# Kernel optimization log

Measured on AMD Instinct MI355X. Metric: run time of the kernel, lower is better.

Reference implementation:

```python
import jax, jax.numpy as jnp
import numpy as np

B, SQ, SK, D, H, DFF = 4, 1024, 1024, 1024, 16, 4096
DEPTH = D // H
EPS = 1e-6


def setup_inputs() -> dict:
    key = jax.random.key(0)
    ks = jax.random.split(key, 32)
    s = 0.02
    inp = {
        "x": jax.random.normal(ks[0], (B, SQ, D), jnp.float32),
        "enc_output": jax.random.normal(ks[1], (B, SK, D), jnp.float32),
        # causal look-ahead mask: 1 where attention is disallowed
        "look_ahead_mask": (1.0 - jnp.tril(jnp.ones((SQ, SQ), jnp.float32)))[None, None],
        "padding_mask": jnp.zeros((B, 1, 1, SK), jnp.float32),
    }
    names = ["wq1", "wk1", "wv1", "wo1", "wq2", "wk2", "wv2", "wo2"]
    for i, n in enumerate(names):
        inp[n] = jax.random.normal(ks[2 + i], (D, D), jnp.float32) * s
        inp["b" + n[1:]] = jnp.zeros((D,), jnp.float32)
    inp["w_ffn1"] = jax.random.normal(ks[12], (D, DFF), jnp.float32) * s
    inp["b_ffn1"] = jnp.zeros((DFF,), jnp.float32)
    inp["w_ffn2"] = jax.random.normal(ks[13], (DFF, D), jnp.float32) * s
    inp["b_ffn2"] = jnp.zeros((D,), jnp.float32)
    for i in (1, 2, 3):
        inp[f"gamma{i}"] = jnp.ones((D,), jnp.float32)
        inp[f"beta{i}"] = jnp.zeros((D,), jnp.float32)
    return inp


def _layernorm(x, gamma, beta):
    mu = jnp.mean(x, axis=-1, keepdims=True)
    var = jnp.var(x, axis=-1, keepdims=True)
    return (x - mu) * jax.lax.rsqrt(var + EPS) * gamma + beta


def _split_heads(x):
    b, s, _ = x.shape
    return x.reshape(b, s, H, DEPTH).transpose(0, 2, 1, 3)  # (B,H,S,depth)


def _mha(v_in, k_in, q_in, mask, wq, bq, wk, bk, wv, bv, wo, bo):
    q = _split_heads(q_in @ wq + bq)
    k = _split_heads(k_in @ wk + bk)
    v = _split_heads(v_in @ wv + bv)
    logits = jnp.einsum("bhqd,bhkd->bhqk", q, k) / jnp.sqrt(jnp.float32(DEPTH))
    if mask is not None:
        logits = logits + mask * -1e9
    attn = jax.nn.softmax(logits, axis=-1)
    out = jnp.einsum("bhqk,bhkd->bhqd", attn, v)
    out = out.transpose(0, 2, 1, 3).reshape(q_in.shape[0], -1, D)
    return out @ wo + bo, attn


def reference(x, enc_output, look_ahead_mask, padding_mask,
              wq1, bq1, wk1, bk1, wv1, bv1, wo1, bo1,
              wq2, bq2, wk2, bk2, wv2, bv2, wo2, bo2,
              w_ffn1, b_ffn1, w_ffn2, b_ffn2,
              gamma1, beta1, gamma2, beta2, gamma3, beta3):
    attn1, aw1 = _mha(x, x, x, look_ahead_mask,
                      wq1, bq1, wk1, bk1, wv1, bv1, wo1, bo1)
    out1 = _layernorm(attn1 + x, gamma1, beta1)
    attn2, aw2 = _mha(enc_output, enc_output, out1, padding_mask,
                      wq2, bq2, wk2, bk2, wv2, bv2, wo2, bo2)
    out2 = _layernorm(attn2 + out1, gamma2, beta2)
    ffn = jax.nn.relu(out2 @ w_ffn1 + b_ffn1) @ w_ffn2 + b_ffn2
    out3 = _layernorm(ffn + out2, gamma3, beta3)
    return out3, aw1, aw2
```

## Files before the change

kernel.cpp:

```cpp
#include <hip/hip_runtime.h>

#define NB 4
#define SEQ 1024
#define DM 1024
#define NH 16
#define DEP 64
#define DFFN 4096

typedef __attribute__((ext_vector_type(8))) short short8;
typedef __attribute__((ext_vector_type(4))) float f32x4;
typedef __attribute__((ext_vector_type(4))) unsigned short us4;

__device__ __forceinline__ unsigned short f2bf(float f) {
    union { float f; unsigned int u; } v; v.f = f;
    unsigned int u = v.u;
    return (unsigned short)((u + 0x7FFFu + ((u >> 16) & 1u)) >> 16);
}

__device__ __forceinline__ void gload16(const void* g, void* l) {
    __builtin_amdgcn_global_load_lds((const __attribute__((address_space(1))) unsigned int*)g,
                                     (__attribute__((address_space(3))) unsigned int*)l, 16, 0, 0);
}

__global__ __launch_bounds__(256) void cast2_kernel(const float* __restrict__ a,
                                                    const float* __restrict__ b,
                                                    unsigned short* __restrict__ oa,
                                                    unsigned short* __restrict__ ob, int n4) {
    int i = blockIdx.x * 256 + threadIdx.x;
    const float* in = blockIdx.y ? b : a;
    unsigned short* out = blockIdx.y ? ob : oa;
    if (i < n4) {
        float4 f = ((const float4*)in)[i];
        us4 u;
        u[0] = f2bf(f.x); u[1] = f2bf(f.y); u[2] = f2bf(f.z); u[3] = f2bf(f.w);
        ((us4*)out)[i] = u;
    }
}

__global__ __launch_bounds__(256) void castT_kernel(const float* __restrict__ in,
                                                    unsigned short* __restrict__ out,
                                                    int R, int C) {
    __shared__ float tile[64][65];
    const int t = threadIdx.x;
    const int c0 = blockIdx.x * 64, r0 = blockIdx.y * 64;
#pragma unroll
    for (int p = 0; p < 4; ++p) {
        int r = p * 16 + (t >> 4), c = (t & 15) * 4;
        float4 f = *(const float4*)(in + (size_t)(r0 + r) * C + c0 + c);
        tile[r][c] = f.x; tile[r][c + 1] = f.y; tile[r][c + 2] = f.z; tile[r][c + 3] = f.w;
    }
    __syncthreads();
#pragma unroll
    for (int p = 0; p < 4; ++p) {
        int n = p * 16 + (t >> 4), k = (t & 15) * 4;
        us4 u;
#pragma unroll
        for (int j = 0; j < 4; ++j) u[j] = f2bf(tile[k + j][n]);
        *(us4*)(out + (size_t)(c0 + n) * R + r0 + k) = u;
    }
}

struct P8 { const float* p[8]; };
__global__ __launch_bounds__(256) void castT8_kernel(P8 srcs, unsigned short* __restrict__ dstbase) {
    __shared__ float tile[64][65];
    const float* in = srcs.p[blockIdx.z];
    unsigned short* out = dstbase + (size_t)blockIdx.z * DM * DM;
    const int t = threadIdx.x;
    const int c0 = blockIdx.x * 64, r0 = blockIdx.y * 64;
#pragma unroll
    for (int p = 0; p < 4; ++p) {
        int r = p * 16 + (t >> 4), c = (t & 15) * 4;
        float4 f = *(const float4*)(in + (size_t)(r0 + r) * DM + c0 + c);
        tile[r][c] = f.x; tile[r][c + 1] = f.y; tile[r][c + 2] = f.z; tile[r][c + 3] = f.w;
    }
    __syncthreads();
#pragma unroll
    for (int p = 0; p < 4; ++p) {
        int n = p * 16 + (t >> 4), k = (t & 15) * 4;
        us4 u;
#pragma unroll
        for (int j = 0; j < 4; ++j) u[j] = f2bf(tile[k + j][n]);
        *(us4*)(out + (size_t)(c0 + n) * DM + r0 + k) = u;
    }
}

__global__ __launch_bounds__(256) void biaspack_kernel(const float* __restrict__ bq1,
                                                       const float* __restrict__ bk1,
                                                       const float* __restrict__ bv1,
                                                       const float* __restrict__ bk2,
                                                       const float* __restrict__ bv2,
                                                       float* __restrict__ bqkv1,
                                                       float* __restrict__ bkv2) {
    int i = blockIdx.x * 256 + threadIdx.x;
    if (i < 1024) bqkv1[i] = bq1[i];
    else if (i < 2048) bqkv1[i] = bk1[i - 1024];
    else if (i < 3072) bqkv1[i] = bv1[i - 2048];
    else if (i < 4096) bkv2[i - 3072] = bk2[i - 3072];
    else if (i < 5120) bkv2[i - 3072] = bv2[i - 4096];
}

template <int BM, int BN, int BK, int KSPLIT, int RELU, int WB, int WF, int WVT>
__global__ __launch_bounds__(256) void gemm_kernel(const unsigned short* __restrict__ A,
                                                   const unsigned short* __restrict__ Wt,
                                                   const float* __restrict__ bias,
                                                   unsigned short* __restrict__ Cb,
                                                   float* __restrict__ Cf,
                                                   float* __restrict__ Cf2,
                                                   unsigned short* __restrict__ Vt,
                                                   int vstart,
                                                   int M, int N, int K) {
    constexpr int AM = BM / 32;
    constexpr int KS = BK / 32;
    constexpr int LPR = BK / 8;
    constexpr int RPI = 64 / LPR;
    constexpr int AR = (BM / 4) / RPI;
    constexpr int BR = (BN / 4) / RPI;
    __shared__ unsigned short As[BM * BK];
    __shared__ unsigned short Bs[BN * BK];
    const int t = threadIdx.x;
    const int lane = t & 63, w = t >> 6;
    const int m0 = blockIdx.y * BM, n0 = blockIdx.x * BN;
    const int wm = (w >> 1) * (BM / 2), wn = (w & 1) * (BN / 2);
    const int lr = lane & 15, g = lane >> 4, kb = g * 8;
    const int srow = lane / LPR, scol = (lane % LPR) * 8;
    const int kofs = (KSPLIT == 2 && blockIdx.z) ? K / 2 : 0;
    const int Keff = (KSPLIT == 2) ? K / 2 : K;

    f32x4 acc[AM][4];
#pragma unroll
    for (int a = 0; a < AM; ++a)
#pragma unroll
        for (int b = 0; b < 4; ++b)
#pragma unroll
            for (int j = 0; j < 4; ++j) acc[a][b][j] = 0.f;

    for (int kt = 0; kt < Keff; kt += BK) {
        __syncthreads();
#pragma unroll
        for (int ia = 0; ia < AR; ++ia) {
            int rb = w * (BM / 4) + ia * RPI;
            gload16(A + (size_t)(m0 + rb + srow) * K + kofs + kt + scol, As + rb * BK);
        }
#pragma unroll
        for (int ib = 0; ib < BR; ++ib) {
            int rb = w * (BN / 4) + ib * RPI;
            gload16(Wt + (size_t)(n0 + rb + srow) * K + kofs + kt + scol, Bs + rb * BK);
        }
        __syncthreads();

        short8 af[AM][KS], bfr[4][KS];
#pragma unroll
        for (int i = 0; i < AM; ++i)
#pragma unroll
            for (int ks = 0; ks < KS; ++ks)
                af[i][ks] = *(const short8*)&As[(wm + i * 16 + lr) * BK + ks * 32 + kb];
#pragma unroll
        for (int i = 0; i < 4; ++i)
#pragma unroll
            for (int ks = 0; ks < KS; ++ks)
                bfr[i][ks] = *(const short8*)&Bs[(wn + i * 16 + lr) * BK + ks * 32 + kb];
#pragma unroll
        for (int ks = 0; ks < KS; ++ks)
#pragma unroll
            for (int am = 0; am < AM; ++am)
#pragma unroll
                for (int bn = 0; bn < 4; ++bn)
                    acc[am][bn] = __builtin_amdgcn_mfma_f32_16x16x32_bf16(af[am][ks], bfr[bn][ks], acc[am][bn], 0, 0, 0);
    }

    float* cfo = (KSPLIT == 2 && blockIdx.z) ? Cf2 : Cf;
    const bool addb = bias && (KSPLIT == 1 || blockIdx.z == 0);
#pragma unroll
    for (int am = 0; am < AM; ++am) {
#pragma unroll
        for (int bn = 0; bn < 4; ++bn) {
            int col = n0 + wn + bn * 16 + lr;
            float bv = addb ? bias[col] : 0.f;
            int rowb = m0 + wm + am * 16 + g * 4;
            float vv[4];
#pragma unroll
            for (int i = 0; i < 4; ++i) {
                float v = acc[am][bn][i] + bv;
                if (RELU) v = v > 0.f ? v : 0.f;
                vv[i] = v;
                if (WF) cfo[(size_t)(rowb + i) * N + col] = v;
                if (WB) Cb[(size_t)(rowb + i) * N + col] = f2bf(v);
            }
            if (WVT && col >= vstart) {
                int h = (col - vstart) >> 6, dep = (col - vstart) & 63;
                int b = rowb >> 10, kpos = rowb & 1023;
                us4 u;
#pragma unroll
                for (int i = 0; i < 4; ++i) u[i] = f2bf(vv[i]);
                *(us4*)(Vt + ((size_t)(b * NH + h) * DEP + dep) * SEQ + kpos) = u;
            }
        }
    }
}

template <int CAUSAL>
__global__ __launch_bounds__(256, 2) void attn_kernel(const unsigned short* __restrict__ Q, int ldq,
                                                      const unsigned short* __restrict__ Kp, int ldk,
                                                      const unsigned short* __restrict__ Vt,
                                                      const float* __restrict__ pad,
                                                      float* __restrict__ aw,
                                                      unsigned short* __restrict__ ctx) {
    __shared__ unsigned short Ks[256 * 64];
    __shared__ unsigned short Pch[32 * 256];
    __shared__ float redm[4][32];
    __shared__ float reds[4][32];
    const int t = threadIdx.x, lane = t & 63, w = t >> 6;
    const int lr = lane & 15, g = lane >> 4;
    const int id = blockIdx.x;
    const int bh = (id & 7) + ((id >> 8) << 3);
    const int qt = (id >> 3) & 31;
    const int q0 = qt * 32;
    const int b = bh >> 4, h = bh & 15;
    const size_t qbase = (size_t)b * SEQ * ldq + (size_t)h * DEP;
    const size_t kbase = (size_t)b * SEQ * ldk + (size_t)h * DEP;
    const int kcmax = CAUSAL ? ((q0 + 16) >> 8) + 1 : 4;

    short8 aq[2][2];
#pragma unroll
    for (int p = 0; p < 2; ++p)
#pragma unroll
        for (int ks = 0; ks < 2; ++ks)
            aq[p][ks] = *(const short8*)(Q + qbase + (size_t)(q0 + p * 16 + lr) * ldq + ks * 32 + g * 8);

    f32x4 acc[2][4][4];
#pragma unroll
    for (int p = 0; p < 2; ++p)
#pragma unroll
        for (int a = 0; a < 4; ++a)
#pragma unroll
            for (int b2 = 0; b2 < 4; ++b2)
#pragma unroll
                for (int j = 0; j < 4; ++j) acc[p][a][b2][j] = 0.f;

    const int srow = lane >> 3;
    const int sslot = (lane & 7) ^ srow;

#pragma unroll
    for (int kc = 0; kc < 4; ++kc) {
        if (kc < kcmax) {
            __syncthreads();
#pragma unroll
            for (int i = 0; i < 8; ++i) {
                int rb = w * 64 + i * 8;
                gload16(Kp + kbase + (size_t)(kc * 256 + rb + srow) * ldk + sslot * 8,
                        Ks + rb * 64);
            }
            __syncthreads();
#pragma unroll
            for (int ks = 0; ks < 2; ++ks)
#pragma unroll
                for (int bn = 0; bn < 4; ++bn) {
                    int row = w * 64 + bn * 16 + lr;
                    short8 bk = *(const short8*)((const char*)Ks + row * 128 +
                                                 ((ks * 64 + g * 16) ^ ((lr & 7) << 4)));
                    acc[0][kc][bn] = __builtin_amdgcn_mfma_f32_16x16x32_bf16(bk, aq[0][ks], acc[0][kc][bn], 0, 0, 0);
                    acc[1][kc][bn] = __builtin_amdgcn_mfma_f32_16x16x32_bf16(bk, aq[1][ks], acc[1][kc][bn], 0, 0, 0);
                }
        }
    }

    float mrow[2] = {-1e30f, -1e30f};
#pragma unroll
    for (int kc = 0; kc < 4; ++kc) {
        if (kc < kcmax) {
#pragma unroll
            for (int bn = 0; bn < 4; ++bn) {
                int k4 = kc * 256 + w * 64 + bn * 16 + g * 4;
                f32x4 pv = {0.f, 0.f, 0.f, 0.f};
                if (pad) pv = *(const f32x4*)(pad + (size_t)b * SEQ + k4);
#pragma unroll
                for (int p = 0; p < 2; ++p) {
                    int q = q0 + p * 16 + lr;
#pragma unroll
                    for (int i = 0; i < 4; ++i) {
                        float v = acc[p][kc][bn][i] * 0.125f + pv[i] * -1e9f;
                        if (CAUSAL && (k4 + i) > q) v = -1e30f;
                        acc[p][kc][bn][i] = v;
                        mrow[p] = fmaxf(mrow[p], v);
                    }
                }
            }
        }
    }
#pragma unroll
    for (int p = 0; p < 2; ++p) {
        mrow[p] = fmaxf(mrow[p], __shfl_xor(mrow[p], 16));
        mrow[p] = fmaxf(mrow[p], __shfl_xor(mrow[p], 32));
    }
    if (lane < 16) { redm[w][lr] = mrow[0]; redm[w][16 + lr] = mrow[1]; }
    __syncthreads();
    float Mv[2];
#pragma unroll
    for (int p = 0; p < 2; ++p)
        Mv[p] = fmaxf(fmaxf(redm[0][p * 16 + lr], redm[1][p * 16 + lr]),
                      fmaxf(redm[2][p * 16 + lr], redm[3][p * 16 + lr]));

    float srw[2] = {0.f, 0.f};
#pragma unroll
    for (int kc = 0; kc < 4; ++kc) {
        if (kc < kcmax) {
#pragma unroll
            for (int p = 0; p < 2; ++p)
#pragma unroll
                for (int bn = 0; bn < 4; ++bn)
#pragma unroll
                    for (int i = 0; i < 4; ++i) {
                        float e = __expf(acc[p][kc][bn][i] - Mv[p]);
                        acc[p][kc][bn][i] = e;
                        srw[p] += e;
                    }
        }
    }
#pragma unroll
    for (int p = 0; p < 2; ++p) {
        srw[p] += __shfl_xor(srw[p], 16);
        srw[p] += __shfl_xor(srw[p], 32);
    }
    if (lane < 16) { reds[w][lr] = srw[0]; reds[w][16 + lr] = srw[1]; }
    __syncthreads();
    float inv[2];
#pragma unroll
    for (int p = 0; p < 2; ++p)
        inv[p] = 1.0f / (reds[0][p * 16 + lr] + reds[1][p * 16 + lr] +
                         reds[2][p * 16 + lr] + reds[3][p * 16 + lr]);

#pragma unroll
    for (int p = 0; p < 2; ++p) {
        float* awrow = aw + ((size_t)bh * SEQ + q0 + p * 16 + lr) * SEQ;
#pragma unroll
        for (int kc = 0; kc < 4; ++kc)
#pragma unroll
            for (int bn = 0; bn < 4; ++bn) {
                f32x4 o = {0.f, 0.f, 0.f, 0.f};
                if (kc < kcmax) {
#pragma unroll
                    for (int i = 0; i < 4; ++i) o[i] = acc[p][kc][bn][i] * inv[p];
                }
                *(f32x4*)(awrow + kc * 256 + w * 64 + bn * 16 + g * 4) = o;
            }
    }

    f32x4 acc2[2];
#pragma unroll
    for (int p = 0; p < 2; ++p)
#pragma unroll
        for (int j = 0; j < 4; ++j) acc2[p][j] = 0.f;
    char* pch = (char*)Pch;
    const int sw = (lr & 7) << 4;
#pragma unroll
    for (int kc = 0; kc < 4; ++kc) {
        if (kc < kcmax) {
            __syncthreads();
#pragma unroll
            for (int p = 0; p < 2; ++p)
#pragma unroll
                for (int bn = 0; bn < 4; ++bn) {
                    us4 u;
#pragma unroll
                    for (int i = 0; i < 4; ++i) u[i] = f2bf(acc[p][kc][bn][i] * inv[p]);
                    *(us4*)(pch + (p * 16 + lr) * 512 + ((w * 128 + bn * 32 + g * 8) ^ sw)) = u;
                }
            __syncthreads();
#pragma unroll
            for (int ks = 0; ks < 8; ++ks) {
                short8 bf = *(const short8*)(Vt + ((size_t)bh * DEP + w * 16 + lr) * SEQ + kc * 256 + ks * 32 + g * 8);
#pragma unroll
                for (int p = 0; p < 2; ++p) {
                    short8 af = *(const short8*)(pch + (p * 16 + lr) * 512 + ((ks * 64 + g * 16) ^ sw));
                    acc2[p] = __builtin_amdgcn_mfma_f32_16x16x32_bf16(af, bf, acc2[p], 0, 0, 0);
                }
            }
        }
    }
#pragma unroll
    for (int p = 0; p < 2; ++p)
#pragma unroll
        for (int i = 0; i < 4; ++i)
            ctx[((size_t)b * SEQ + q0 + p * 16 + g * 4 + i) * DM + h * DEP + w * 16 + lr] = f2bf(acc2[p][i]);
}

template <int WB, int X2EN>
__global__ __launch_bounds__(256) void ln_kernel(const float* __restrict__ X,
                                                 const float* __restrict__ X2,
                                                 const float* __restrict__ R,
                                                 const float* __restrict__ gamma,
                                                 const float* __restrict__ beta,
                                                 float* __restrict__ outF,
                                                 unsigned short* __restrict__ outB) {
    size_t row = blockIdx.x;
    const int t = threadIdx.x;
    float4 a = ((const float4*)(X + (row << 10)))[t];
    float4 r = ((const float4*)(R + (row << 10)))[t];
    float v0 = a.x + r.x, v1 = a.y + r.y, v2 = a.z + r.z, v3 = a.w + r.w;
    if (X2EN) {
        float4 a2 = ((const float4*)(X2 + (row << 10)))[t];
        v0 += a2.x; v1 += a2.y; v2 += a2.z; v3 += a2.w;
    }
    float s = v0 + v1 + v2 + v3;
    float q = v0 * v0 + v1 * v1 + v2 * v2 + v3 * v3;
#pragma unroll
    for (int off = 32; off; off >>= 1) {
        s += __shfl_down(s, off);
        q += __shfl_down(q, off);
    }
    __shared__ float rs[4], rq[4];
    if ((t & 63) == 0) { rs[t >> 6] = s; rq[t >> 6] = q; }
    __syncthreads();
    s = rs[0] + rs[1] + rs[2] + rs[3];
    q = rq[0] + rq[1] + rq[2] + rq[3];
    float mean = s * (1.0f / 1024.0f);
    float var = q * (1.0f / 1024.0f) - mean * mean;
    float inv = rsqrtf(var + 1e-6f);
    float g0 = gamma[t * 4], g1 = gamma[t * 4 + 1], g2 = gamma[t * 4 + 2], g3 = gamma[t * 4 + 3];
    float b0 = beta[t * 4], b1 = beta[t * 4 + 1], b2 = beta[t * 4 + 2], b3 = beta[t * 4 + 3];
    float o0 = (v0 - mean) * inv * g0 + b0;
    float o1 = (v1 - mean) * inv * g1 + b1;
    float o2 = (v2 - mean) * inv * g2 + b2;
    float o3 = (v3 - mean) * inv * g3 + b3;
    float4 o; o.x = o0; o.y = o1; o.z = o2; o.w = o3;
    ((float4*)(outF + (row << 10)))[t] = o;
    if (WB) {
        us4 u;
        u[0] = f2bf(o0); u[1] = f2bf(o1); u[2] = f2bf(o2); u[3] = f2bf(o3);
        ((us4*)(outB + (row << 10)))[t] = u;
    }
}

extern "C" void kernel_launch(void* const* d_in, const int* in_sizes, int n_in,
                              void* d_out, int out_size, void* d_ws, size_t ws_size,
                              hipStream_t stream) {
    const float* x = (const float*)d_in[0];
    const float* enc = (const float*)d_in[1];
    const float* pad = (const float*)d_in[3];
    const float* wq1 = (const float*)d_in[4];  const float* bq1 = (const float*)d_in[5];
    const float* wk1 = (const float*)d_in[6];  const float* bk1 = (const float*)d_in[7];
    const float* wv1 = (const float*)d_in[8];  const float* bv1 = (const float*)d_in[9];
    const float* wo1 = (const float*)d_in[10]; const float* bo1 = (const float*)d_in[11];
    const float* wq2 = (const float*)d_in[12]; const float* bq2 = (const float*)d_in[13];
    const float* wk2 = (const float*)d_in[14]; const float* bk2 = (const float*)d_in[15];
    const float* wv2 = (const float*)d_in[16]; const float* bv2 = (const float*)d_in[17];
    const float* wo2 = (const float*)d_in[18]; const float* bo2 = (const float*)d_in[19];
    const float* wf1 = (const float*)d_in[20]; const float* bf1 = (const float*)d_in[21];
    const float* wf2 = (const float*)d_in[22]; const float* bf2 = (const float*)d_in[23];
    const float* g1 = (const float*)d_in[24]; const float* be1 = (const float*)d_in[25];
    const float* g2 = (const float*)d_in[26]; const float* be2 = (const float*)d_in[27];
    const float* g3 = (const float*)d_in[28]; const float* be3 = (const float*)d_in[29];

    float* out3 = (float*)d_out;
    float* aw1 = out3 + (size_t)NB * SEQ * DM;
    float* aw2 = aw1 + (size_t)NB * NH * SEQ * SEQ;

    char* ws = (char*)d_ws;
    size_t off = 0;
    auto take = [&](size_t n) { char* p = ws + off; off += (n + 255) & ~(size_t)255; return p; };
    const size_t SZ_SD_BF = (size_t)NB * SEQ * DM * 2;
    const size_t SZ_SD_F  = (size_t)NB * SEQ * DM * 4;
    const size_t SZ_DD_BF = (size_t)DM * DM * 2;

    unsigned short* wqkv1t = (unsigned short*)take(3 * SZ_DD_BF);
    unsigned short* wq2t   = (unsigned short*)take(SZ_DD_BF);
    unsigned short* wkv2t  = (unsigned short*)take(2 * SZ_DD_BF);
    unsigned short* wo1t   = (unsigned short*)take(SZ_DD_BF);
    unsigned short* wo2t   = (unsigned short*)take(SZ_DD_BF);
    unsigned short* wf1t   = (unsigned short*)take((size_t)DM * DFFN * 2);
    unsigned short* wf2t   = (unsigned short*)take((size_t)DFFN * DM * 2);
    float* bqkv1 = (float*)take(3 * DM * 4);
    float* bkv2  = (float*)take(2 * DM * 4);
    unsigned short* xb    = (unsigned short*)take(SZ_SD_BF);
    unsigned short* encb  = (unsigned short*)take(SZ_SD_BF);
    unsigned short* qkv1b = (unsigned short*)take(3 * SZ_SD_BF);
    unsigned short* v1t   = (unsigned short*)take(SZ_SD_BF);
    unsigned short* qb    = (unsigned short*)take(SZ_SD_BF);
    unsigned short* kv2b  = (unsigned short*)take(2 * SZ_SD_BF);
    unsigned short* v2t   = (unsigned short*)take(SZ_SD_BF);
    unsigned short* ctx   = (unsigned short*)take(SZ_SD_BF);
    float* goutf  = (float*)take(SZ_SD_F);
    float* gout2f = (float*)take(SZ_SD_F);
    float* out1f  = (float*)take(SZ_SD_F);
    unsigned short* out1b = (unsigned short*)take(SZ_SD_BF);
    float* out2f  = (float*)take(SZ_SD_F);
    unsigned short* out2b = (unsigned short*)take(SZ_SD_BF);
    unsigned short* ffn1b = (unsigned short*)take((size_t)NB * SEQ * DFFN * 2);

    {
        int n4 = NB * SEQ * DM / 4;
        dim3 gc((n4 + 255) / 256, 2);
        cast2_kernel<<<gc, 256, 0, stream>>>(x, enc, xb, encb, n4);
    }
    {
        P8 s;
        s.p[0] = wq1; s.p[1] = wk1; s.p[2] = wv1; s.p[3] = wq2;
        s.p[4] = wk2; s.p[5] = wv2; s.p[6] = wo1; s.p[7] = wo2;
        dim3 g8(DM / 64, DM / 64, 8);
        castT8_kernel<<<g8, 256, 0, stream>>>(s, wqkv1t);
    }
    castT_kernel<<<dim3(DFFN / 64, DM / 64), 256, 0, stream>>>(wf1, wf1t, DM, DFFN);
    castT_kernel<<<dim3(DM / 64, DFFN / 64), 256, 0, stream>>>(wf2, wf2t, DFFN, DM);
    biaspack_kernel<<<20, 256, 0, stream>>>(bq1, bk1, bv1, bk2, bv2, bqkv1, bkv2);

    const int M = NB * SEQ;
    dim3 gQKV(3 * DM / 128, M / 128);
    dim3 gKV(2 * DM / 128, M / 128);
    dim3 gDD64(DM / 128, M / 64);
    dim3 gDF(DFFN / 128, M / 128);
    dim3 gF2(DM / 128, M / 128, 2);

    gemm_kernel<128, 128, 32, 1, 0, 1, 0, 1><<<gQKV, 256, 0, stream>>>(xb, wqkv1t, bqkv1, qkv1b, nullptr, nullptr, v1t, 2048, M, 3 * DM, DM);
    attn_kernel<1><<<2048, 256, 0, stream>>>(qkv1b, 3 * DM, qkv1b + DM, 3 * DM, v1t, nullptr, aw1, ctx);
    gemm_kernel<64, 128, 64, 1, 0, 0, 1, 0><<<gDD64, 256, 0, stream>>>(ctx, wo1t, bo1, nullptr, goutf, nullptr, nullptr, 0, M, DM, DM);
    ln_kernel<1, 0><<<M, 256, 0, stream>>>(goutf, nullptr, x, g1, be1, out1f, out1b);

    gemm_kernel<64, 128, 64, 1, 0, 1, 0, 0><<<gDD64, 256, 0, stream>>>(out1b, wq2t, bq2, qb, nullptr, nullptr, nullptr, 0, M, DM, DM);
    gemm_kernel<128, 128, 32, 1, 0, 1, 0, 1><<<gKV, 256, 0, stream>>>(encb, wkv2t, bkv2, kv2b, nullptr, nullptr, v2t, 1024, M, 2 * DM, DM);
    attn_kernel<0><<<2048, 256, 0, stream>>>(qb, DM, kv2b, 2 * DM, v2t, pad, aw2, ctx);
    gemm_kernel<64, 128, 64, 1, 0, 0, 1, 0><<<gDD64, 256, 0, stream>>>(ctx, wo2t, bo2, nullptr, goutf, nullptr, nullptr, 0, M, DM, DM);
    ln_kernel<1, 0><<<M, 256, 0, stream>>>(goutf, nullptr, out1f, g2, be2, out2f, out2b);

    gemm_kernel<128, 128, 32, 1, 1, 1, 0, 0><<<gDF, 256, 0, stream>>>(out2b, wf1t, bf1, ffn1b, nullptr, nullptr, nullptr, 0, M, DFFN, DM);
    gemm_kernel<128, 128, 32, 2, 0, 0, 1, 0><<<gF2, 256, 0, stream>>>(ffn1b, wf2t, bf2, nullptr, goutf, gout2f, nullptr, 0, M, DM, DFFN);
    ln_kernel<0, 1><<<M, 256, 0, stream>>>(goutf, gout2f, out2f, g3, be3, out3, nullptr);
}
```

Baseline: 579.3 us.

## Double-buffer K tiles in attention, merge weight casts, widen GEMM K tile

The attention kernel now walks K in 128-key chunks with two LDS buffers, prefetching the next chunk while MFMAs run on the current one. This drops one barrier per chunk and gives finer causal skipping. The three weight transpose-cast launches are merged into a single kernel. The large GEMMs use a K-tile of 64 instead of 32 to halve main-loop iterations. The costs are more LDS per GEMM block, which may lower occupancy, and more accumulator bookkeeping in attention.

New measurement: 590.5 us. Within noise of the previous version (+1.9%).

```diff
diff --git a/kernel.cpp b/kernel.cpp
--- a/kernel.cpp
+++ b/kernel.cpp
@@ -37,12 +37,27 @@
     }
 }
 
-__global__ __launch_bounds__(256) void castT_kernel(const float* __restrict__ in,
-                                                    unsigned short* __restrict__ out,
-                                                    int R, int C) {
+struct P10 { const float* p[10]; };
+__global__ __launch_bounds__(256) void castTall_kernel(P10 s,
+                                                       unsigned short* __restrict__ wsq,
+                                                       unsigned short* __restrict__ wf1t,
+                                                       unsigned short* __restrict__ wf2t) {
     __shared__ float tile[64][65];
-    const int t = threadIdx.x;
-    const int c0 = blockIdx.x * 64, r0 = blockIdx.y * 64;
+    const int tid = blockIdx.x, t = threadIdx.x;
+    const float* in; unsigned short* out; int R, C, r0, c0;
+    if (tid < 2048) {
+        int wi = tid >> 8, t2 = tid & 255;
+        in = s.p[wi]; out = wsq + (size_t)wi * DM * DM; R = DM; C = DM;
+        r0 = (t2 >> 4) * 64; c0 = (t2 & 15) * 64;
+    } else if (tid < 3072) {
+        int t2 = tid - 2048;
+        in = s.p[8]; out = wf1t; R = DM; C = DFFN;
+        r0 = (t2 >> 6) * 64; c0 = (t2 & 63) * 64;
+    } else {
+        int t2 = tid - 3072;
+        in = s.p[9]; out = wf2t; R = DFFN; C = DM;
+        r0 = (t2 >> 4) * 64; c0 = (t2 & 15) * 64;
+    }
 #pragma unroll
     for (int p = 0; p < 4; ++p) {
         int r = p * 16 + (t >> 4), c = (t & 15) * 4;
@@ -57,30 +72,6 @@
 #pragma unroll
         for (int j = 0; j < 4; ++j) u[j] = f2bf(tile[k + j][n]);
         *(us4*)(out + (size_t)(c0 + n) * R + r0 + k) = u;
-    }
-}
-
-struct P8 { const float* p[8]; };
-__global__ __launch_bounds__(256) void castT8_kernel(P8 srcs, unsigned short* __restrict__ dstbase) {
-    __shared__ float tile[64][65];
-    const float* in = srcs.p[blockIdx.z];
-    unsigned short* out = dstbase + (size_t)blockIdx.z * DM * DM;
-    const int t = threadIdx.x;
-    const int c0 = blockIdx.x * 64, r0 = blockIdx.y * 64;
-#pragma unroll
-    for (int p = 0; p < 4; ++p) {
-        int r = p * 16 + (t >> 4), c = (t & 15) * 4;
-        float4 f = *(const float4*)(in + (size_t)(r0 + r) * DM + c0 + c);
-        tile[r][c] = f.x; tile[r][c + 1] = f.y; tile[r][c + 2] = f.z; tile[r][c + 3] = f.w;
-    }
-    __syncthreads();
-#pragma unroll
-    for (int p = 0; p < 4; ++p) {
-        int n = p * 16 + (t >> 4), k = (t & 15) * 4;
-        us4 u;
-#pragma unroll
-        for (int j = 0; j < 4; ++j) u[j] = f2bf(tile[k + j][n]);
-        *(us4*)(out + (size_t)(c0 + n) * DM + r0 + k) = u;
     }
 }
 
@@ -205,8 +196,8 @@
                                                       const float* __restrict__ pad,
                                                       float* __restrict__ aw,
                                                       unsigned short* __restrict__ ctx) {
-    __shared__ unsigned short Ks[256 * 64];
-    __shared__ unsigned short Pch[32 * 256];
+    __shared__ unsigned short Ks[2][128 * 64];
+    __shared__ unsigned short Pch[32 * 128];
     __shared__ float redm[4][32];
     __shared__ float reds[4][32];
     const int t = threadIdx.x, lane = t & 63, w = t >> 6;
@@ -218,7 +209,10 @@
     const int b = bh >> 4, h = bh & 15;
     const size_t qbase = (size_t)b * SEQ * ldq + (size_t)h * DEP;
     const size_t kbase = (size_t)b * SEQ * ldk + (size_t)h * DEP;
-    const int kcmax = CAUSAL ? ((q0 + 16) >> 8) + 1 : 4;
+    const int cmax = CAUSAL ? (q0 >> 7) + 1 : 8;
+
+    const int srow = lane >> 3;
+    const int sslot = (lane & 7) ^ srow;
 
     short8 aq[2][2];
 #pragma unroll
@@ -227,50 +221,55 @@
         for (int ks = 0; ks < 2; ++ks)
             aq[p][ks] = *(const short8*)(Q + qbase + (size_t)(q0 + p * 16 + lr) * ldq + ks * 32 + g * 8);
 
-    f32x4 acc[2][4][4];
+    f32x4 acc[2][8][2];
 #pragma unroll
     for (int p = 0; p < 2; ++p)
 #pragma unroll
-        for (int a = 0; a < 4; ++a)
-#pragma unroll
-            for (int b2 = 0; b2 < 4; ++b2)
-#pragma unroll
-                for (int j = 0; j < 4; ++j) acc[p][a][b2][j] = 0.f;
-
-    const int srow = lane >> 3;
-    const int sslot = (lane & 7) ^ srow;
-
-#pragma unroll
-    for (int kc = 0; kc < 4; ++kc) {
-        if (kc < kcmax) {
+        for (int c = 0; c < 8; ++c)
+#pragma unroll
+            for (int bn = 0; bn < 2; ++bn)
+#pragma unroll
+                for (int j = 0; j < 4; ++j) acc[p][c][bn][j] = 0.f;
+
+    {
+#pragma unroll
+        for (int i = 0; i < 4; ++i) {
+            int rb = w * 32 + i * 8;
+            gload16(Kp + kbase + (size_t)(0 * 128 + rb + srow) * ldk + sslot * 8, &Ks[0][rb * 64]);
+        }
+    }
+#pragma unroll
+    for (int c = 0; c < 8; ++c) {
+        if (c < cmax) {
             __syncthreads();
-#pragma unroll
-            for (int i = 0; i < 8; ++i) {
-                int rb = w * 64 + i * 8;
-                gload16(Kp + kbase + (size_t)(kc * 256 + rb + srow) * ldk + sslot * 8,
-                        Ks + rb * 64);
+            if (c + 1 < cmax) {
+#pragma unroll
+                for (int i = 0; i < 4; ++i) {
+                    int rb = w * 32 + i * 8;
+                    gload16(Kp + kbase + (size_t)((c + 1) * 128 + rb + srow) * ldk + sslot * 8,
+                            &Ks[(c + 1) & 1][rb * 64]);
+                }
             }
-            __syncthreads();
 #pragma unroll
             for (int ks = 0; ks < 2; ++ks)
 #pragma unroll
-                for (int bn = 0; bn < 4; ++bn) {
-                    int row = w * 64 + bn * 16 + lr;
-                    short8 bk = *(const short8*)((const char*)Ks + row * 128 +
+                for (int bn = 0; bn < 2; ++bn) {
+                    int row = w * 32 + bn * 16 + lr;
+                    short8 bk = *(const short8*)((const char*)&Ks[c & 1][0] + row * 128 +
                                                  ((ks * 64 + g * 16) ^ ((lr & 7) << 4)));
-                    acc[0][kc][bn] = __builtin_amdgcn_mfma_f32_16x16x32_bf16(bk, aq[0][ks], acc[0][kc][bn], 0, 0, 0);
-                    acc[1][kc][bn] = __builtin_amdgcn_mfma_f32_16x16x32_bf16(bk, aq[1][ks], acc[1][kc][bn], 0, 0, 0);
+                    acc[0][c][bn] = __builtin_amdgcn_mfma_f32_16x16x32_bf16(bk, aq[0][ks], acc[0][c][bn], 0, 0, 0);
+                    acc[1][c][bn] = __builtin_amdgcn_mfma_f32_16x16x32_bf16(bk, aq[1][ks], acc[1][c][bn], 0, 0, 0);
                 }
         }
     }
 
     float mrow[2] = {-1e30f, -1e30f};
 #pragma unroll
-    for (int kc = 0; kc < 4; ++kc) {
-        if (kc < kcmax) {
-#pragma unroll
-            for (int bn = 0; bn < 4; ++bn) {
-                int k4 = kc * 256 + w * 64 + bn * 16 + g * 4;
+    for (int c = 0; c < 8; ++c) {
+        if (c < cmax) {
+#pragma unroll
+            for (int bn = 0; bn < 2; ++bn) {
+                int k4 = c * 128 + w * 32 + bn * 16 + g * 4;
                 f32x4 pv = {0.f, 0.f, 0.f, 0.f};
                 if (pad) pv = *(const f32x4*)(pad + (size_t)b * SEQ + k4);
 #pragma unroll
@@ -278,9 +277,9 @@
                     int q = q0 + p * 16 + lr;
 #pragma unroll
                     for (int i = 0; i < 4; ++i) {
-                        float v = acc[p][kc][bn][i] * 0.125f + pv[i] * -1e9f;
+                        float v = acc[p][c][bn][i] * 0.125f + pv[i] * -1e9f;
                         if (CAUSAL && (k4 + i) > q) v = -1e30f;
-                        acc[p][kc][bn][i] = v;
+                        acc[p][c][bn][i] = v;
                         mrow[p] = fmaxf(mrow[p], v);
                     }
                 }
@@ -302,16 +301,16 @@
 
     float srw[2] = {0.f, 0.f};
 #pragma unroll
-    for (int kc = 0; kc < 4; ++kc) {
-        if (kc < kcmax) {
+    for (int c = 0; c < 8; ++c) {
+        if (c < cmax) {
 #pragma unroll
             for (int p = 0; p < 2; ++p)
 #pragma unroll
-                for (int bn = 0; bn < 4; ++bn)
+                for (int bn = 0; bn < 2; ++bn)
 #pragma unroll
                     for (int i = 0; i < 4; ++i) {
-                        float e = __expf(acc[p][kc][bn][i] - Mv[p]);
-                        acc[p][kc][bn][i] = e;
+                        float e = __expf(acc[p][c][bn][i] - Mv[p]);
+                        acc[p][c][bn][i] = e;
                         srw[p] += e;
                     }
         }
@@ -333,15 +332,15 @@
     for (int p = 0; p < 2; ++p) {
         float* awrow = aw + ((size_t)bh * SEQ + q0 + p * 16 + lr) * SEQ;
 #pragma unroll
-        for (int kc = 0; kc < 4; ++kc)
-#pragma unroll
-            for (int bn = 0; bn < 4; ++bn) {
+        for (int c = 0; c < 8; ++c)
+#pragma unroll
+            for (int bn = 0; bn < 2; ++bn) {
                 f32x4 o = {0.f, 0.f, 0.f, 0.f};
-                if (kc < kcmax) {
-#pragma unroll
-                    for (int i = 0; i < 4; ++i) o[i] = acc[p][kc][bn][i] * inv[p];
+                if (c < cmax) {
+#pragma unroll
+                    for (int i = 0; i < 4; ++i) o[i] = acc[p][c][bn][i] * inv[p];
                 }
-                *(f32x4*)(awrow + kc * 256 + w * 64 + bn * 16 + g * 4) = o;
+                *(f32x4*)(awrow + c * 128 + w * 32 + bn * 16 + g * 4) = o;
             }
     }
 
@@ -353,25 +352,25 @@
     char* pch = (char*)Pch;
     const int sw = (lr & 7) << 4;
 #pragma unroll
-    for (int kc = 0; kc < 4; ++kc) {
-        if (kc < kcmax) {
+    for (int c = 0; c < 8; ++c) {
+        if (c < cmax) {
             __syncthreads();
 #pragma unroll
             for (int p = 0; p < 2; ++p)
 #pragma unroll
-                for (int bn = 0; bn < 4; ++bn) {
+                for (int bn = 0; bn < 2; ++bn) {
                     us4 u;
 #pragma unroll
-                    for (int i = 0; i < 4; ++i) u[i] = f2bf(acc[p][kc][bn][i] * inv[p]);
-                    *(us4*)(pch + (p * 16 + lr) * 512 + ((w * 128 + bn * 32 + g * 8) ^ sw)) = u;
+                    for (int i = 0; i < 4; ++i) u[i] = f2bf(acc[p][c][bn][i] * inv[p]);
+                    *(us4*)(pch + (p * 16 + lr) * 256 + ((w * 64 + bn * 32 + g * 8) ^ sw)) = u;
                 }
             __syncthreads();
 #pragma unroll
-            for (int ks = 0; ks < 8; ++ks) {
-                short8 bf = *(const short8*)(Vt + ((size_t)bh * DEP + w * 16 + lr) * SEQ + kc * 256 + ks * 32 + g * 8);
+            for (int ks = 0; ks < 4; ++ks) {
+                short8 bf = *(const short8*)(Vt + ((size_t)bh * DEP + w * 16 + lr) * SEQ + c * 128 + ks * 32 + g * 8);
 #pragma unroll
                 for (int p = 0; p < 2; ++p) {
-                    short8 af = *(const short8*)(pch + (p * 16 + lr) * 512 + ((ks * 64 + g * 16) ^ sw));
+                    short8 af = *(const short8*)(pch + (p * 16 + lr) * 256 + ((ks * 64 + g * 16) ^ sw));
                     acc2[p] = __builtin_amdgcn_mfma_f32_16x16x32_bf16(af, bf, acc2[p], 0, 0, 0);
                 }
             }
@@ -493,14 +492,12 @@
         cast2_kernel<<<gc, 256, 0, stream>>>(x, enc, xb, encb, n4);
     }
     {
-        P8 s;
+        P10 s;
         s.p[0] = wq1; s.p[1] = wk1; s.p[2] = wv1; s.p[3] = wq2;
         s.p[4] = wk2; s.p[5] = wv2; s.p[6] = wo1; s.p[7] = wo2;
-        dim3 g8(DM / 64, DM / 64, 8);
-        castT8_kernel<<<g8, 256, 0, stream>>>(s, wqkv1t);
-    }
-    castT_kernel<<<dim3(DFFN / 64, DM / 64), 256, 0, stream>>>(wf1, wf1t, DM, DFFN);
-    castT_kernel<<<dim3(DM / 64, DFFN / 64), 256, 0, stream>>>(wf2, wf2t, DFFN, DM);
+        s.p[8] = wf1; s.p[9] = wf2;
+        castTall_kernel<<<4096, 256, 0, stream>>>(s, wqkv1t, wf1t, wf2t);
+    }
     biaspack_kernel<<<20, 256, 0, stream>>>(bq1, bk1, bv1, bk2, bv2, bqkv1, bkv2);
 
     const int M = NB * SEQ;
@@ -510,18 +507,18 @@
     dim3 gDF(DFFN / 128, M / 128);
     dim3 gF2(DM / 128, M / 128, 2);
 
-    gemm_kernel<128, 128, 32, 1, 0, 1, 0, 1><<<gQKV, 256, 0, stream>>>(xb, wqkv1t, bqkv1, qkv1b, nullptr, nullptr, v1t, 2048, M, 3 * DM, DM);
+    gemm_kernel<128, 128, 64, 1, 0, 1, 0, 1><<<gQKV, 256, 0, stream>>>(xb, wqkv1t, bqkv1, qkv1b, nullptr, nullptr, v1t, 2048, M, 3 * DM, DM);
     attn_kernel<1><<<2048, 256, 0, stream>>>(qkv1b, 3 * DM, qkv1b + DM, 3 * DM, v1t, nullptr, aw1, ctx);
     gemm_kernel<64, 128, 64, 1, 0, 0, 1, 0><<<gDD64, 256, 0, stream>>>(ctx, wo1t, bo1, nullptr, goutf, nullptr, nullptr, 0, M, DM, DM);
     ln_kernel<1, 0><<<M, 256, 0, stream>>>(goutf, nullptr, x, g1, be1, out1f, out1b);
 
     gemm_kernel<64, 128, 64, 1, 0, 1, 0, 0><<<gDD64, 256, 0, stream>>>(out1b, wq2t, bq2, qb, nullptr, nullptr, nullptr, 0, M, DM, DM);
-    gemm_kernel<128, 128, 32, 1, 0, 1, 0, 1><<<gKV, 256, 0, stream>>>(encb, wkv2t, bkv2, kv2b, nullptr, nullptr, v2t, 1024, M, 2 * DM, DM);
+    gemm_kernel<128, 128, 64, 1, 0, 1, 0, 1><<<gKV, 256, 0, stream>>>(encb, wkv2t, bkv2, kv2b, nullptr, nullptr, v2t, 1024, M, 2 * DM, DM);
     attn_kernel<0><<<2048, 256, 0, stream>>>(qb, DM, kv2b, 2 * DM, v2t, pad, aw2, ctx);
     gemm_kernel<64, 128, 64, 1, 0, 0, 1, 0><<<gDD64, 256, 0, stream>>>(ctx, wo2t, bo2, nullptr, goutf, nullptr, nullptr, 0, M, DM, DM);
     ln_kernel<1, 0><<<M, 256, 0, stream>>>(goutf, nullptr, out1f, g2, be2, out2f, out2b);
 
-    gemm_kernel<128, 128, 32, 1, 1, 1, 0, 0><<<gDF, 256, 0, stream>>>(out2b, wf1t, bf1, ffn1b, nullptr, nullptr, nullptr, 0, M, DFFN, DM);
-    gemm_kernel<128, 128, 32, 2, 0, 0, 1, 0><<<gF2, 256, 0, stream>>>(ffn1b, wf2t, bf2, nullptr, goutf, gout2f, nullptr, 0, M, DM, DFFN);
+    gemm_kernel<128, 128, 64, 1, 1, 1, 0, 0><<<gDF, 256, 0, stream>>>(out2b, wf1t, bf1, ffn1b, nullptr, nullptr, nullptr, 0, M, DFFN, DM);
+    gemm_kernel<128, 128, 64, 2, 0, 0, 1, 0><<<gF2, 256, 0, stream>>>(ffn1b, wf2t, bf2, nullptr, goutf, gout2f, nullptr, 0, M, DM, DFFN);
     ln_kernel<0, 1><<<M, 256, 0, stream>>>(goutf, gout2f, out2f, g3, be3, out3, nullptr);
 }
```
